# Optimization experiments

Hardware: AMD Instinct MI355X
Metric: run time of the kernel (lower is better)

## Reference

```python
import jax, jax.numpy as jnp
import numpy as np
from math import sqrt

BASE = 10000.0  # rope_theta
NUM_HEADS = 16


def _quant(x):
    # per-row (last-dim) symmetric int8 fake-quant, matching ActivationQuantSTE.forward
    scale = 127.0 / jnp.maximum(jnp.max(jnp.abs(x), axis=-1, keepdims=True), 1e-5)
    return jnp.clip(jnp.round(x * scale), -128.0, 127.0) / scale


@jax.custom_vjp
def act_quant(x):
    return _quant(x)

def _aq_fwd(x):
    return _quant(x), None

def _aq_bwd(_, g):
    return (g,)  # straight-through estimator

act_quant.defvjp(_aq_fwd, _aq_bwd)


def complex_linear(xr, xi, Wr, Wi):
    # ComplexLinearBase: quantize activations, then
    #   y_real = q_real @ Wr^T + q_imag @ Wi^T
    #   y_imag = q_real @ Wi^T - q_imag @ Wr^T
    qr = act_quant(xr)
    qi = act_quant(xi)
    yr = qr @ Wr.T + qi @ Wi.T
    yi = qr @ Wi.T - qi @ Wr.T
    return yr, yi


def setup_inputs() -> dict:
    T, H = 2048, 2048
    key = jax.random.key(0)
    ks = jax.random.split(key, 10)
    w = lambda k: jax.random.normal(k, (H, H), jnp.float32) * 0.02
    return {
        "hidden_real": jax.random.normal(ks[0], (T, H), jnp.float32),
        "hidden_imag": jax.random.normal(ks[1], (T, H), jnp.float32),
        "positions": jnp.arange(T, dtype=jnp.int32),
        "Wq_r": w(ks[2]), "Wq_i": w(ks[3]),
        "Wk_r": w(ks[4]), "Wk_i": w(ks[5]),
        "Wv_r": w(ks[6]), "Wv_i": w(ks[7]),
        "Wo_r": w(ks[8]), "Wo_i": w(ks[9]),
    }


def reference(hidden_real, hidden_imag, positions, Wq_r, Wq_i, Wk_r, Wk_i, Wv_r, Wv_i, Wo_r, Wo_i):
    T, H = hidden_real.shape
    NH = NUM_HEADS
    D = H // NH  # head_dim

    # complex QKV projections with int8 activation fake-quant
    qr, qi = complex_linear(hidden_real, hidden_imag, Wq_r, Wq_i)
    kr, ki = complex_linear(hidden_real, hidden_imag, Wk_r, Wk_i)
    vr, vi = complex_linear(hidden_real, hidden_imag, Wv_r, Wv_i)

    # Complex RoPE: interleaving (real, imag) then GPT-J-style rotation with
    # head_size = rotary_dim = 2*D is equivalent to rotating (real, imag) pairs:
    #   out_real = real*cos - imag*sin ; out_imag = imag*cos + real*sin
    # inv_freq = base^-(arange(0, 2D, 2)/(2D)) = base^-(arange(D)/D), len D.
    inv_freq = 1.0 / (BASE ** (jnp.arange(D, dtype=jnp.float32) / D))
    freqs = positions.astype(jnp.float32)[:, None] * inv_freq[None, :]  # [T, D]
    # cache is stored in bf16 in the original module
    cos = jnp.cos(freqs).astype(jnp.bfloat16).astype(jnp.float32)[:, None, :]  # [T,1,D]
    sin = jnp.sin(freqs).astype(jnp.bfloat16).astype(jnp.float32)[:, None, :]

    def rope(xr_, xi_):
        r = xr_.reshape(T, NH, D)
        i = xi_.reshape(T, NH, D)
        return r * cos - i * sin, i * cos + r * sin

    qr3, qi3 = rope(qr, qi)
    kr3, ki3 = rope(kr, ki)
    vr3 = vr.reshape(T, NH, D)
    vi3 = vi.reshape(T, NH, D)

    # causal attention; scores = Re(q . conj(k)) / sqrt(2*D)  (complex dim is 2*D)
    scale = 1.0 / sqrt(2 * D)
    scores = (jnp.einsum('thd,shd->hts', qr3, kr3)
              + jnp.einsum('thd,shd->hts', qi3, ki3)) * scale  # [NH, T, T]
    causal = jnp.tril(jnp.ones((T, T), dtype=bool))
    scores = jnp.where(causal[None], scores, -1e9)
    p = jax.nn.softmax(scores, axis=-1)

    out_r = jnp.einsum('hts,shd->thd', p, vr3).reshape(T, H)
    out_i = jnp.einsum('hts,shd->thd', p, vi3).reshape(T, H)

    # complex output projection (with activation fake-quant)
    return complex_linear(out_r, out_i, Wo_r, Wo_i)
```

## Files before the change

kernel.cpp:

```cpp
#include <hip/hip_runtime.h>


typedef float v4f __attribute__((ext_vector_type(4)));
typedef _Float16 v8h __attribute__((ext_vector_type(8)));
typedef _Float16 v4h __attribute__((ext_vector_type(4)));

typedef const __attribute__((address_space(1))) void glob_void;
typedef __attribute__((address_space(3))) void lds_void;

__device__ __forceinline__ void gload16(const _Float16* gp, _Float16* lp) {
  __builtin_amdgcn_global_load_lds((glob_void*)gp, (lds_void*)lp, 16, 0, 0);
}

__device__ __forceinline__ float bf16_rt(float f) {
  union { float f; unsigned u; } a; a.f = f;
  unsigned r = (a.u + 0x7fffu + ((a.u >> 16) & 1u)) & 0xffff0000u;
  union { unsigned u; float f; } b; b.u = r;
  return b.f;
}

#define EPI_QKV 0
#define EPI_OUT 1

#define SBAR()  __builtin_amdgcn_sched_barrier(0)
#define WBAR()  __builtin_amdgcn_s_barrier()
#define LGKM0() asm volatile("s_waitcnt lgkmcnt(0)" ::: "memory")
#define LDS_BARRIER() do { SBAR(); LGKM0(); WBAR(); SBAR(); } while (0)

__global__ __launch_bounds__(512, 2) void gemm_qkv256(
    const _Float16* __restrict__ A, const _Float16* __restrict__ B,
    _Float16* __restrict__ Yq, _Float16* __restrict__ vt)
{
  const int p = blockIdx.x;
  const int xcd = p & 7, s = p >> 3;
  const int mt = s & 7, ntl = s >> 3;
  const int nt = xcd * 8 + ntl;
  const int m0 = mt << 8;
  const int n0 = nt * 192;

  __shared__ __align__(16) _Float16 lds[57344];

  const int tid = threadIdx.x, lane = tid & 63, wave = tid >> 6;
  const int quad = lane >> 4, l15 = lane & 15;
  const int wm = wave >> 2, wn = wave & 3;

  const int rr = tid >> 2;
  const int lc8 = (((tid & 3) ^ ((tid >> 3) & 3)) << 3);
  const _Float16* gA = A + (long long)(m0 + rr) * 4096 + lc8;
  const _Float16* gBj[3];
#pragma unroll
  for (int j = 0; j < 3; ++j) {
    const int ks = (j == 2) || (j == 1 && tid >= 256);
    const int r = j * 128 + (tid >> 2) - ks * 192;
    gBj[j] = B + (long long)(n0 + r) * 4096 + ks * 32 + lc8;
  }

  const int co = ((quad ^ ((l15 >> 1) & 3)) << 3);
  const int aBase = (wm * 128 + l15) * 32 + co;
  const int bBase = (wn * 48 + l15) * 32 + co;

  v4f acc[8][3] = {};

  {
    _Float16* sd = lds + tid * 8;
    gload16(gA, sd);
    gload16(gA + 524288, sd + 4096);
    gload16(gBj[0], sd + 16384);
    gload16(gBj[1], sd + 20480);
    gload16(gA + 32, sd + 8192);
    gload16(gA + 524288 + 32, sd + 12288);
    gload16(gBj[2], sd + 24576);
  }
  asm volatile("s_waitcnt vmcnt(3)" ::: "memory");
  WBAR();

  for (int t = 0; t < 64; ++t) {
    const _Float16* As = lds + (t & 1) * 28672;
    const _Float16* Bs = As + 16384;
    _Float16* sd = lds + ((t & 1) ^ 1) * 28672 + tid * 8;
    const int k1 = (t + 1) << 6;
    const bool stg = (t < 63);

    v8h bf[3], af[4];

    af[0] = *(const v8h*)&As[aBase];
    af[1] = *(const v8h*)&As[aBase + 512];
    af[2] = *(const v8h*)&As[aBase + 1024];
    af[3] = *(const v8h*)&As[aBase + 1536];
    bf[0] = *(const v8h*)&Bs[bBase];
    bf[1] = *(const v8h*)&Bs[bBase + 512];
    bf[2] = *(const v8h*)&Bs[bBase + 1024];
    if (stg) { gload16(gA + k1, sd); gload16(gA + k1 + 524288, sd + 4096); }
    SBAR(); WBAR(); LGKM0(); SBAR();
    __builtin_amdgcn_s_setprio(1);
#pragma unroll
    for (int i = 0; i < 4; ++i)
#pragma unroll
      for (int nf = 0; nf < 3; ++nf)
        acc[i][nf] = __builtin_amdgcn_mfma_f32_16x16x32_f16(af[i], bf[nf], acc[i][nf], 0, 0, 0);
    __builtin_amdgcn_s_setprio(0);
    WBAR();

    af[0] = *(const v8h*)&As[aBase + 2048];
    af[1] = *(const v8h*)&As[aBase + 2560];
    af[2] = *(const v8h*)&As[aBase + 3072];
    af[3] = *(const v8h*)&As[aBase + 3584];
    if (stg) { gload16(gBj[0] + k1, sd + 16384); gload16(gBj[1] + k1, sd + 20480); }
    SBAR(); WBAR(); LGKM0(); SBAR();
    __builtin_amdgcn_s_setprio(1);
#pragma unroll
    for (int i = 0; i < 4; ++i)
#pragma unroll
      for (int nf = 0; nf < 3; ++nf)
        acc[4 + i][nf] = __builtin_amdgcn_mfma_f32_16x16x32_f16(af[i], bf[nf], acc[4 + i][nf], 0, 0, 0);
    __builtin_amdgcn_s_setprio(0);
    if (stg) asm volatile("s_waitcnt vmcnt(4)" ::: "memory");
    else     asm volatile("s_waitcnt vmcnt(0)" ::: "memory");
    WBAR();

    bf[0] = *(const v8h*)&Bs[bBase + 6144];
    bf[1] = *(const v8h*)&Bs[bBase + 6656];
    bf[2] = *(const v8h*)&Bs[bBase + 7168];
    af[0] = *(const v8h*)&As[aBase + 8192];
    af[1] = *(const v8h*)&As[aBase + 8704];
    af[2] = *(const v8h*)&As[aBase + 9216];
    af[3] = *(const v8h*)&As[aBase + 9728];
    if (stg) { gload16(gA + k1 + 32, sd + 8192); gload16(gA + k1 + 524288 + 32, sd + 12288); }
    SBAR(); WBAR(); LGKM0(); SBAR();
    __builtin_amdgcn_s_setprio(1);
#pragma unroll
    for (int i = 0; i < 4; ++i)
#pragma unroll
      for (int nf = 0; nf < 3; ++nf)
        acc[i][nf] = __builtin_amdgcn_mfma_f32_16x16x32_f16(af[i], bf[nf], acc[i][nf], 0, 0, 0);
    __builtin_amdgcn_s_setprio(0);
    WBAR();

    af[0] = *(const v8h*)&As[aBase + 10240];
    af[1] = *(const v8h*)&As[aBase + 10752];
    af[2] = *(const v8h*)&As[aBase + 11264];
    af[3] = *(const v8h*)&As[aBase + 11776];
    if (stg) gload16(gBj[2] + k1, sd + 24576);
    SBAR(); WBAR(); LGKM0(); SBAR();
    __builtin_amdgcn_s_setprio(1);
#pragma unroll
    for (int i = 0; i < 4; ++i)
#pragma unroll
      for (int nf = 0; nf < 3; ++nf)
        acc[4 + i][nf] = __builtin_amdgcn_mfma_f32_16x16x32_f16(af[i], bf[nf], acc[4 + i][nf], 0, 0, 0);
    __builtin_amdgcn_s_setprio(0);
    if (stg) asm volatile("s_waitcnt vmcnt(3)" ::: "memory");
    WBAR();
  }

#pragma unroll
  for (int mf = 0; mf < 8; ++mf) {
#pragma unroll
    for (int nf = 0; nf < 3; ++nf) {
      const int col = n0 + wn * 48 + nf * 16 + l15;
      const int row0 = m0 + wm * 128 + mf * 16 + quad * 4;
      if (col >= 8192) {
        const int c = col - 8192;
        const int hh = (c & 2047) >> 7;
        const int dcol = (c < 2048) ? (c & 127) : (128 + (c & 127));
        v4h pk;
#pragma unroll
        for (int r = 0; r < 4; ++r) pk[r] = (_Float16)acc[mf][nf][r];
        *(v4h*)(vt + ((long long)(hh * 256 + dcol)) * 2048 + row0) = pk;
      } else {
#pragma unroll
        for (int r = 0; r < 4; ++r)
          Yq[(long long)(row0 + r) * 8192 + col] = (_Float16)acc[mf][nf][r];
      }
    }
  }
}

template<int EPI>
__global__ __launch_bounds__(256) void gemm_nt(
    const _Float16* __restrict__ A, const _Float16* __restrict__ B,
    void* __restrict__ Cv, int K, int lda, int ldb, int ldc,
    _Float16* __restrict__ vtout)
{
  const int m0 = blockIdx.x * 128, n0 = blockIdx.y * 128;

  __shared__ __align__(16) _Float16 As[128 * 32];
  __shared__ __align__(16) _Float16 Bs[128 * 32];

  const int tid = threadIdx.x, lane = tid & 63, wave = tid >> 6;
  const int off0 = tid * 8, off1 = 2048 + tid * 8;
  const int r0 = off0 >> 5, r1 = off1 >> 5;
  const int c0 = ((((off0 >> 3) & 3) ^ ((r0 >> 1) & 3)) << 3);
  const int c1 = ((((off1 >> 3) & 3) ^ ((r1 >> 1) & 3)) << 3);
  const _Float16* ga0 = A + (long long)(m0 + r0) * lda + c0;
  const _Float16* ga1 = A + (long long)(m0 + r1) * lda + c1;
  const _Float16* gb0 = B + (long long)(n0 + r0) * ldb + c0;
  const _Float16* gb1 = B + (long long)(n0 + r1) * ldb + c1;

  const int mr = (wave >> 1) * 64 + (lane & 15);
  const int nr = (wave & 1) * 64 + (lane & 15);
  const int kq = lane >> 4;

  v4f acc[4][4] = {};

  for (int k0 = 0; k0 < K; k0 += 32) {
    gload16(ga0 + k0, As + off0);
    gload16(ga1 + k0, As + off1);
    gload16(gb0 + k0, Bs + off0);
    gload16(gb1 + k0, Bs + off1);
    __syncthreads();
    v8h a[4], b[4];
#pragma unroll
    for (int i = 0; i < 4; ++i) {
      const int r = mr + i * 16;
      a[i] = *(const v8h*)&As[r * 32 + ((kq ^ ((r >> 1) & 3)) << 3)];
    }
#pragma unroll
    for (int j = 0; j < 4; ++j) {
      const int r = nr + j * 16;
      b[j] = *(const v8h*)&Bs[r * 32 + ((kq ^ ((r >> 1) & 3)) << 3)];
    }
#pragma unroll
    for (int i = 0; i < 4; ++i)
#pragma unroll
      for (int j = 0; j < 4; ++j)
        acc[i][j] = __builtin_amdgcn_mfma_f32_16x16x32_f16(a[i], b[j], acc[i][j], 0, 0, 0);
    __syncthreads();
  }

  const int cr = (wave >> 1) * 64 + (lane >> 4) * 4;
  const int cc = (wave & 1) * 64 + (lane & 15);
#pragma unroll
  for (int i = 0; i < 4; ++i)
#pragma unroll
    for (int j = 0; j < 4; ++j) {
      const int col = n0 + cc + j * 16;
      if (EPI == EPI_QKV && col >= 8192) {
        const int c = col - 8192;
        const int hh = (c & 2047) >> 7;
        const int dcol = (c < 2048) ? (c & 127) : (128 + (c & 127));
        const int row0 = m0 + cr + i * 16;
        v4h pk;
#pragma unroll
        for (int r = 0; r < 4; ++r) pk[r] = (_Float16)acc[i][j][r];
        *(v4h*)(vtout + ((long long)(hh * 256 + dcol)) * 2048 + row0) = pk;
      } else {
#pragma unroll
        for (int r = 0; r < 4; ++r) {
          const int row = m0 + cr + i * 16 + r;
          const float v = acc[i][j][r];
          if (EPI == EPI_QKV) {
            ((_Float16*)Cv)[(long long)row * ldc + col] = (_Float16)v;
          } else {
            float* O = (float*)Cv;
            if (col < 2048) O[(long long)row * 2048 + col] = v;
            else O[2048ll * 2048 + (long long)row * 2048 + (col - 2048)] = v;
          }
        }
      }
    }
}

__global__ __launch_bounds__(256) void quant_rows(
    const float* __restrict__ s0, const float* __restrict__ s1,
    _Float16* __restrict__ dst)
{
  const int t = blockIdx.x, y = blockIdx.y;
  const float* src = (y ? s1 : s0) + (long long)t * 2048;
  const int tid = threadIdx.x, lane = tid & 63, wave = tid >> 6;
  __shared__ float rbuf[4];
  const v4f a = *(const v4f*)(src + tid * 4);
  const v4f b = *(const v4f*)(src + 1024 + tid * 4);
  float m = 0.f;
#pragma unroll
  for (int k = 0; k < 4; ++k)
    m = fmaxf(m, fmaxf(fabsf(a[k]), fabsf(b[k])));
  for (int o = 1; o < 64; o <<= 1) m = fmaxf(m, __shfl_xor(m, o, 64));
  if (lane == 0) rbuf[wave] = m;
  __syncthreads();
  m = fmaxf(fmaxf(rbuf[0], rbuf[1]), fmaxf(rbuf[2], rbuf[3]));
  const float scale = 127.f / fmaxf(m, 1e-5f);
  const float inv = 1.f / scale;
  _Float16* d = dst + (long long)t * 4096 + (long long)y * 2048 + tid * 4;
  v4h qa, qb;
#pragma unroll
  for (int k = 0; k < 4; ++k) {
    qa[k] = (_Float16)(fminf(fmaxf(rintf(a[k] * scale), -128.f), 127.f) * inv);
    qb[k] = (_Float16)(fminf(fmaxf(rintf(b[k] * scale), -128.f), 127.f) * inv);
  }
  *(v4h*)d = qa;
  *(v4h*)(d + 1024) = qb;
}

__global__ __launch_bounds__(256) void wprep(
    const float* __restrict__ Wq_r, const float* __restrict__ Wq_i,
    const float* __restrict__ Wk_r, const float* __restrict__ Wk_i,
    const float* __restrict__ Wv_r, const float* __restrict__ Wv_i,
    const float* __restrict__ Wo_r, const float* __restrict__ Wo_i,
    _Float16* __restrict__ Bqkv, _Float16* __restrict__ Bo)
{
  const float* Ws[8] = {Wq_r, Wq_i, Wk_r, Wk_i, Wv_r, Wv_i, Wo_r, Wo_i};
  const int i = blockIdx.x * 256 + threadIdx.x;
  const int w = i >> 18;
  const int rem = i & 262143;
  const int j = rem >> 7;
  const int cb = (rem & 127) * 16;
  const float* src = Ws[w] + (long long)j * 2048 + cb;
  _Float16* Bp = (w < 6) ? (Bqkv + (long long)(w >> 1) * 4096 * 4096) : Bo;
  const int isI = w & 1;
  _Float16* d1 = Bp + (long long)j * 4096 + (isI ? 2048 + cb : cb);
  _Float16* d2 = Bp + (long long)(2048 + j) * 4096 + (isI ? cb : 2048 + cb);
  const float sg2 = isI ? 1.f : -1.f;
#pragma unroll
  for (int q = 0; q < 4; ++q) {
    const v4f v = *(const v4f*)(src + q * 4);
    v4h o1, o2;
#pragma unroll
    for (int k = 0; k < 4; ++k) {
      o1[k] = (_Float16)v[k];
      o2[k] = (_Float16)(v[k] * sg2);
    }
    *(v4h*)(d1 + q * 4) = o1;
    *(v4h*)(d2 + q * 4) = o2;
  }
}

__global__ __launch_bounds__(256) void trig_kernel(
    const int* __restrict__ pos, float* __restrict__ cs)
{
  const int t = blockIdx.x * 2 + (threadIdx.x >> 7);
  const int d = threadIdx.x & 127;
  const float invf = (float)pow(10000.0, -(double)d / 128.0);
  const float fr = (float)pos[t] * invf;
  const double fd = (double)fr;
  cs[((long long)t * 128 + d) * 2]     = bf16_rt((float)cos(fd));
  cs[((long long)t * 128 + d) * 2 + 1] = bf16_rt((float)sin(fd));
}

__global__ __launch_bounds__(256) void rope_kernel(
    const _Float16* __restrict__ Yq, const float* __restrict__ cs,
    _Float16* __restrict__ qc, _Float16* __restrict__ kc)
{
  const int idx = blockIdx.x * 256 + threadIdx.x;
  const int d0 = (idx & 15) * 8;
  const int h  = (idx >> 4) & 15;
  const int t  = idx >> 8;
  const _Float16* y = Yq + (long long)t * 8192 + h * 128 + d0;
  const v8h qr8 = *(const v8h*)(y);
  const v8h qi8 = *(const v8h*)(y + 2048);
  const v8h kr8 = *(const v8h*)(y + 4096);
  const v8h ki8 = *(const v8h*)(y + 6144);
  const float* cp = cs + ((long long)t * 128 + d0) * 2;
  v8h qro, qio, kro, kio;
#pragma unroll
  for (int u = 0; u < 8; ++u) {
    const float c = cp[u * 2], s = cp[u * 2 + 1];
    const float qr = (float)qr8[u], qi = (float)qi8[u];
    const float kr = (float)kr8[u], ki = (float)ki8[u];
    qro[u] = (_Float16)(qr * c - qi * s);
    qio[u] = (_Float16)(qi * c + qr * s);
    kro[u] = (_Float16)(kr * c - ki * s);
    kio[u] = (_Float16)(ki * c + kr * s);
  }
  _Float16* qo = qc + ((long long)h * 2048 + t) * 256 + d0;
  _Float16* ko = kc + ((long long)h * 2048 + t) * 256 + d0;
  *(v8h*)qo = qro; *(v8h*)(qo + 128) = qio;
  *(v8h*)ko = kro; *(v8h*)(ko + 128) = kio;
}

__global__ __launch_bounds__(256, 2) void flash_attn(
    const _Float16* __restrict__ qc, const _Float16* __restrict__ kc,
    const _Float16* __restrict__ vt, float* __restrict__ attn)
{
  __shared__ __align__(16) _Float16 Ps[64 * 72];
  __shared__ float pmax[2][64];
  __shared__ float psum[2][64];

  const int h  = blockIdx.y;
  const int qt = ((h >> 3) & 1) ? (31 - (int)blockIdx.x) : (int)blockIdx.x;
  const int q0 = qt * 64;
  const int tid = threadIdx.x, lane = tid & 63, wave = tid >> 6;
  const int mi = wave >> 1, ni = wave & 1;
  const int quad = lane >> 4, l15 = lane & 15;

  const _Float16* qh = qc + (long long)h * 2048 * 256;
  const _Float16* kh = kc + (long long)h * 2048 * 256;
  const _Float16* vh = vt + (long long)h * 256 * 2048;

  const _Float16 scl = (_Float16)0.09016844f;
  v8h qf[2][8];
#pragma unroll
  for (int mt = 0; mt < 2; ++mt) {
    const int t = q0 + mi * 32 + mt * 16 + l15;
#pragma unroll
    for (int ks = 0; ks < 8; ++ks) {
      v8h q = *(const v8h*)(qh + (long long)t * 256 + ks * 32 + quad * 8);
#pragma unroll
      for (int u = 0; u < 8; ++u) q[u] *= scl;
      qf[mt][ks] = q;
    }
  }

  float mrow[2][4], lrow[2][4];
  v4f acc_o[2][8];
#pragma unroll
  for (int mt = 0; mt < 2; ++mt)
#pragma unroll
    for (int r = 0; r < 4; ++r) { mrow[mt][r] = -1e30f; lrow[mt][r] = 0.f; }
#pragma unroll
  for (int mt = 0; mt < 2; ++mt)
#pragma unroll
    for (int nt = 0; nt < 8; ++nt) acc_o[mt][nt] = (v4f){0.f, 0.f, 0.f, 0.f};

  for (int st = 0; st <= qt; ++st) {
    const int s0 = st * 64;

    v4f sa[2][2] = {};
#pragma unroll
    for (int ks = 0; ks < 8; ++ks) {
      v8h bk[2];
#pragma unroll
      for (int jn = 0; jn < 2; ++jn)
        bk[jn] = *(const v8h*)(kh + (long long)(s0 + ni * 32 + jn * 16 + l15) * 256
                               + ks * 32 + quad * 8);
      __builtin_amdgcn_s_setprio(1);
#pragma unroll
      for (int mt = 0; mt < 2; ++mt)
#pragma unroll
        for (int jn = 0; jn < 2; ++jn)
          sa[mt][jn] = __builtin_amdgcn_mfma_f32_16x16x32_f16(qf[mt][ks], bk[jn], sa[mt][jn], 0, 0, 0);
      __builtin_amdgcn_s_setprio(0);
    }

    const bool diag = (st == qt);
    float pm[2][4];
#pragma unroll
    for (int mt = 0; mt < 2; ++mt)
#pragma unroll
      for (int r = 0; r < 4; ++r) pm[mt][r] = -1e30f;
#pragma unroll
    for (int mt = 0; mt < 2; ++mt)
#pragma unroll
      for (int jn = 0; jn < 2; ++jn)
#pragma unroll
        for (int r = 0; r < 4; ++r) {
          float v = sa[mt][jn][r];
          if (diag) {
            const int rl = mi * 32 + mt * 16 + quad * 4 + r;
            const int cl = ni * 32 + jn * 16 + l15;
            if (cl > rl) v = -1e30f;
          }
          sa[mt][jn][r] = v;
          pm[mt][r] = fmaxf(pm[mt][r], v);
        }
#pragma unroll
    for (int o = 1; o < 16; o <<= 1)
#pragma unroll
      for (int mt = 0; mt < 2; ++mt)
#pragma unroll
        for (int r = 0; r < 4; ++r)
          pm[mt][r] = fmaxf(pm[mt][r], __shfl_xor(pm[mt][r], o, 64));
    if (l15 == 0) {
#pragma unroll
      for (int mt = 0; mt < 2; ++mt)
#pragma unroll
        for (int r = 0; r < 4; ++r)
          pmax[ni][mi * 32 + mt * 16 + quad * 4 + r] = pm[mt][r];
    }
    LDS_BARRIER();

    float al[2][4], ps[2][4];
#pragma unroll
    for (int mt = 0; mt < 2; ++mt)
#pragma unroll
      for (int r = 0; r < 4; ++r) {
        const int row = mi * 32 + mt * 16 + quad * 4 + r;
        const float mn = fmaxf(mrow[mt][r], fmaxf(pmax[0][row], pmax[1][row]));
        al[mt][r] = __builtin_amdgcn_exp2f(mrow[mt][r] - mn);
        mrow[mt][r] = mn;
        ps[mt][r] = 0.f;
      }
#pragma unroll
    for (int mt = 0; mt < 2; ++mt)
#pragma unroll
      for (int jn = 0; jn < 2; ++jn)
#pragma unroll
        for (int r = 0; r < 4; ++r) {
          const float e = __builtin_amdgcn_exp2f(sa[mt][jn][r] - mrow[mt][r]);
          ps[mt][r] += e;
          Ps[(mi * 32 + mt * 16 + quad * 4 + r) * 72 + ni * 32 + jn * 16 + l15] = (_Float16)e;
        }
#pragma unroll
    for (int o = 1; o < 16; o <<= 1)
#pragma unroll
      for (int mt = 0; mt < 2; ++mt)
#pragma unroll
        for (int r = 0; r < 4; ++r)
          ps[mt][r] += __shfl_xor(ps[mt][r], o, 64);
    if (l15 == 0) {
#pragma unroll
      for (int mt = 0; mt < 2; ++mt)
#pragma unroll
        for (int r = 0; r < 4; ++r)
          psum[ni][mi * 32 + mt * 16 + quad * 4 + r] = ps[mt][r];
    }
    LDS_BARRIER();

#pragma unroll
    for (int mt = 0; mt < 2; ++mt)
#pragma unroll
      for (int r = 0; r < 4; ++r) {
        const int row = mi * 32 + mt * 16 + quad * 4 + r;
        lrow[mt][r] = lrow[mt][r] * al[mt][r] + psum[0][row] + psum[1][row];
      }
#pragma unroll
    for (int mt = 0; mt < 2; ++mt)
#pragma unroll
      for (int nt = 0; nt < 8; ++nt)
#pragma unroll
        for (int r = 0; r < 4; ++r)
          acc_o[mt][nt][r] *= al[mt][r];

#pragma unroll
    for (int kc2 = 0; kc2 < 2; ++kc2) {
      v8h pa[2];
#pragma unroll
      for (int mt = 0; mt < 2; ++mt) {
        const int row = mi * 32 + mt * 16 + l15;
        pa[mt] = *(const v8h*)(Ps + row * 72 + kc2 * 32 + quad * 8);
      }
#pragma unroll
      for (int nt = 0; nt < 8; ++nt) {
        const v8h vb = *(const v8h*)(vh + (long long)(ni * 128 + nt * 16 + l15) * 2048
                                     + s0 + kc2 * 32 + quad * 8);
        __builtin_amdgcn_s_setprio(1);
#pragma unroll
        for (int mt = 0; mt < 2; ++mt)
          acc_o[mt][nt] = __builtin_amdgcn_mfma_f32_16x16x32_f16(pa[mt], vb, acc_o[mt][nt], 0, 0, 0);
        __builtin_amdgcn_s_setprio(0);
      }
    }
  }

#pragma unroll
  for (int mt = 0; mt < 2; ++mt) {
    float inv[4];
#pragma unroll
    for (int r = 0; r < 4; ++r) inv[r] = 1.f / lrow[mt][r];
#pragma unroll
    for (int nt = 0; nt < 8; ++nt) {
      const int d = ni * 128 + nt * 16 + l15;
      float* dst = attn + ((d < 128) ? 0ll : (2048ll * 2048)) + (h * 128 + (d & 127));
#pragma unroll
      for (int r = 0; r < 4; ++r) {
        const int t = q0 + mi * 32 + mt * 16 + quad * 4 + r;
        dst[(long long)t * 2048] = acc_o[mt][nt][r] * inv[r];
      }
    }
  }
}

extern "C" void kernel_launch(void* const* d_in, const int* in_sizes, int n_in,
                              void* d_out, int out_size, void* d_ws, size_t ws_size,
                              hipStream_t stream) {
  const float* hr   = (const float*)d_in[0];
  const float* hi   = (const float*)d_in[1];
  const int*   pos  = (const int*)d_in[2];
  const float* Wq_r = (const float*)d_in[3];
  const float* Wq_i = (const float*)d_in[4];
  const float* Wk_r = (const float*)d_in[5];
  const float* Wk_i = (const float*)d_in[6];
  const float* Wv_r = (const float*)d_in[7];
  const float* Wv_i = (const float*)d_in[8];
  const float* Wo_r = (const float*)d_in[9];
  const float* Wo_i = (const float*)d_in[10];

  char* ws = (char*)d_ws;
  _Float16* Bqkv = (_Float16*)(ws);
  float*    attn = (float*)   (ws);
  float*    cs   = (float*)   (ws + (32ll  << 20));
  _Float16* Bo   = (_Float16*)(ws + (96ll  << 20));
  _Float16* Ac   = (_Float16*)(ws + (128ll << 20));
  _Float16* Yq   = (_Float16*)(ws + (144ll << 20));
  _Float16* qc   = (_Float16*)(ws + (176ll << 20));
  _Float16* kc   = (_Float16*)(ws + (192ll << 20));
  _Float16* vt   = (_Float16*)(ws + (208ll << 20));

  quant_rows<<<dim3(2048, 2), 256, 0, stream>>>(hr, hi, Ac);
  wprep<<<8192, 256, 0, stream>>>(Wq_r, Wq_i, Wk_r, Wk_i, Wv_r, Wv_i, Wo_r, Wo_i, Bqkv, Bo);
  gemm_qkv256<<<512, 512, 0, stream>>>(Ac, Bqkv, Yq, vt);
  trig_kernel<<<1024, 256, 0, stream>>>(pos, cs);
  rope_kernel<<<2048, 256, 0, stream>>>(Yq, cs, qc, kc);
  flash_attn<<<dim3(32, 16), 256, 0, stream>>>(qc, kc, vt, attn);
  quant_rows<<<dim3(2048, 2), 256, 0, stream>>>(attn, attn + 2048ll * 2048, Ac);
  gemm_nt<EPI_OUT><<<dim3(16, 32), 256, 0, stream>>>(
      Ac, Bo, d_out, 4096, 4096, 4096, 0, nullptr);
}
```

Baseline: 774.1 us.

## Replace output GEMM with double-buffered 256x128 pipelined kernel, simplify attention sync

Replaces the simple single-buffered 128x128 output projection GEMM with a 512-thread, 256x128-tile kernel. It double-buffers LDS and issues async global-to-LDS loads interleaved with MFMA phases, and maps blocks with XCD-aware ordering. This is meant to hide memory latency and improve reuse in the K=4096 output GEMM. Separately, attention drops the s_setprio hints and its custom barrier macro in favour of __syncthreads, which may slightly change scheduling.

```diff
diff --git a/kernel.cpp b/kernel.cpp
--- a/kernel.cpp
+++ b/kernel.cpp
@@ -19,13 +19,9 @@
   return b.f;
 }
 
-#define EPI_QKV 0
-#define EPI_OUT 1
-
 #define SBAR()  __builtin_amdgcn_sched_barrier(0)
 #define WBAR()  __builtin_amdgcn_s_barrier()
 #define LGKM0() asm volatile("s_waitcnt lgkmcnt(0)" ::: "memory")
-#define LDS_BARRIER() do { SBAR(); LGKM0(); WBAR(); SBAR(); } while (0)
 
 __global__ __launch_bounds__(512, 2) void gemm_qkv256(
     const _Float16* __restrict__ A, const _Float16* __restrict__ B,
@@ -176,89 +172,137 @@
   }
 }
 
-template<int EPI>
-__global__ __launch_bounds__(256) void gemm_nt(
+__global__ __launch_bounds__(512, 2) void gemm_out256(
     const _Float16* __restrict__ A, const _Float16* __restrict__ B,
-    void* __restrict__ Cv, int K, int lda, int ldb, int ldc,
-    _Float16* __restrict__ vtout)
+    float* __restrict__ O)
 {
-  const int m0 = blockIdx.x * 128, n0 = blockIdx.y * 128;
-
-  __shared__ __align__(16) _Float16 As[128 * 32];
-  __shared__ __align__(16) _Float16 Bs[128 * 32];
+  const int p = blockIdx.x;
+  const int xcd = p & 7, s = p >> 3;
+  const int mt = s & 7, ntl = s >> 3;
+  const int nt = xcd * 4 + ntl;
+  const int m0 = mt << 8, n0 = nt << 7;
+
+  __shared__ __align__(16) _Float16 lds[49152];
 
   const int tid = threadIdx.x, lane = tid & 63, wave = tid >> 6;
-  const int off0 = tid * 8, off1 = 2048 + tid * 8;
-  const int r0 = off0 >> 5, r1 = off1 >> 5;
-  const int c0 = ((((off0 >> 3) & 3) ^ ((r0 >> 1) & 3)) << 3);
-  const int c1 = ((((off1 >> 3) & 3) ^ ((r1 >> 1) & 3)) << 3);
-  const _Float16* ga0 = A + (long long)(m0 + r0) * lda + c0;
-  const _Float16* ga1 = A + (long long)(m0 + r1) * lda + c1;
-  const _Float16* gb0 = B + (long long)(n0 + r0) * ldb + c0;
-  const _Float16* gb1 = B + (long long)(n0 + r1) * ldb + c1;
-
-  const int mr = (wave >> 1) * 64 + (lane & 15);
-  const int nr = (wave & 1) * 64 + (lane & 15);
-  const int kq = lane >> 4;
-
-  v4f acc[4][4] = {};
-
-  for (int k0 = 0; k0 < K; k0 += 32) {
-    gload16(ga0 + k0, As + off0);
-    gload16(ga1 + k0, As + off1);
-    gload16(gb0 + k0, Bs + off0);
-    gload16(gb1 + k0, Bs + off1);
-    __syncthreads();
-    v8h a[4], b[4];
-#pragma unroll
-    for (int i = 0; i < 4; ++i) {
-      const int r = mr + i * 16;
-      a[i] = *(const v8h*)&As[r * 32 + ((kq ^ ((r >> 1) & 3)) << 3)];
-    }
-#pragma unroll
-    for (int j = 0; j < 4; ++j) {
-      const int r = nr + j * 16;
-      b[j] = *(const v8h*)&Bs[r * 32 + ((kq ^ ((r >> 1) & 3)) << 3)];
-    }
-#pragma unroll
-    for (int i = 0; i < 4; ++i)
-#pragma unroll
-      for (int j = 0; j < 4; ++j)
-        acc[i][j] = __builtin_amdgcn_mfma_f32_16x16x32_f16(a[i], b[j], acc[i][j], 0, 0, 0);
-    __syncthreads();
-  }
-
-  const int cr = (wave >> 1) * 64 + (lane >> 4) * 4;
-  const int cc = (wave & 1) * 64 + (lane & 15);
-#pragma unroll
-  for (int i = 0; i < 4; ++i)
-#pragma unroll
-    for (int j = 0; j < 4; ++j) {
-      const int col = n0 + cc + j * 16;
-      if (EPI == EPI_QKV && col >= 8192) {
-        const int c = col - 8192;
-        const int hh = (c & 2047) >> 7;
-        const int dcol = (c < 2048) ? (c & 127) : (128 + (c & 127));
-        const int row0 = m0 + cr + i * 16;
-        v4h pk;
-#pragma unroll
-        for (int r = 0; r < 4; ++r) pk[r] = (_Float16)acc[i][j][r];
-        *(v4h*)(vtout + ((long long)(hh * 256 + dcol)) * 2048 + row0) = pk;
-      } else {
-#pragma unroll
-        for (int r = 0; r < 4; ++r) {
-          const int row = m0 + cr + i * 16 + r;
-          const float v = acc[i][j][r];
-          if (EPI == EPI_QKV) {
-            ((_Float16*)Cv)[(long long)row * ldc + col] = (_Float16)v;
-          } else {
-            float* O = (float*)Cv;
-            if (col < 2048) O[(long long)row * 2048 + col] = v;
-            else O[2048ll * 2048 + (long long)row * 2048 + (col - 2048)] = v;
-          }
-        }
+  const int quad = lane >> 4, l15 = lane & 15;
+  const int wm = wave >> 2, wn = wave & 3;
+
+  const int rr = tid >> 2;
+  const int lc8 = (((tid & 3) ^ ((tid >> 3) & 3)) << 3);
+  const _Float16* gA = A + (long long)(m0 + rr) * 4096 + lc8;
+  const _Float16* gB = B + (long long)(n0 + rr) * 4096 + lc8;
+
+  const int co = ((quad ^ ((l15 >> 1) & 3)) << 3);
+  const int aBase = (wm * 128 + l15) * 32 + co;
+  const int bBase = (wn * 32 + l15) * 32 + co;
+
+  v4f acc[8][2] = {};
+
+  {
+    _Float16* sd = lds + tid * 8;
+    gload16(gA, sd);
+    gload16(gA + 524288, sd + 4096);
+    gload16(gB, sd + 16384);
+    gload16(gA + 32, sd + 8192);
+    gload16(gA + 524288 + 32, sd + 12288);
+    gload16(gB + 32, sd + 20480);
+  }
+  asm volatile("s_waitcnt vmcnt(3)" ::: "memory");
+  WBAR();
+
+  for (int t = 0; t < 64; ++t) {
+    const _Float16* As = lds + (t & 1) * 24576;
+    const _Float16* Bs = As + 16384;
+    _Float16* sd = lds + ((t & 1) ^ 1) * 24576 + tid * 8;
+    const int k1 = (t + 1) << 6;
+    const bool stg = (t < 63);
+
+    v8h bf[2], af[4];
+
+    af[0] = *(const v8h*)&As[aBase];
+    af[1] = *(const v8h*)&As[aBase + 512];
+    af[2] = *(const v8h*)&As[aBase + 1024];
+    af[3] = *(const v8h*)&As[aBase + 1536];
+    bf[0] = *(const v8h*)&Bs[bBase];
+    bf[1] = *(const v8h*)&Bs[bBase + 512];
+    if (stg) { gload16(gA + k1, sd); gload16(gA + k1 + 524288, sd + 4096); }
+    SBAR(); WBAR(); LGKM0(); SBAR();
+    __builtin_amdgcn_s_setprio(1);
+#pragma unroll
+    for (int i = 0; i < 4; ++i)
+#pragma unroll
+      for (int nf = 0; nf < 2; ++nf)
+        acc[i][nf] = __builtin_amdgcn_mfma_f32_16x16x32_f16(af[i], bf[nf], acc[i][nf], 0, 0, 0);
+    __builtin_amdgcn_s_setprio(0);
+    WBAR();
+
+    af[0] = *(const v8h*)&As[aBase + 2048];
+    af[1] = *(const v8h*)&As[aBase + 2560];
+    af[2] = *(const v8h*)&As[aBase + 3072];
+    af[3] = *(const v8h*)&As[aBase + 3584];
+    if (stg) gload16(gB + k1, sd + 16384);
+    SBAR(); WBAR(); LGKM0(); SBAR();
+    __builtin_amdgcn_s_setprio(1);
+#pragma unroll
+    for (int i = 0; i < 4; ++i)
+#pragma unroll
+      for (int nf = 0; nf < 2; ++nf)
+        acc[4 + i][nf] = __builtin_amdgcn_mfma_f32_16x16x32_f16(af[i], bf[nf], acc[4 + i][nf], 0, 0, 0);
+    __builtin_amdgcn_s_setprio(0);
+    if (stg) asm volatile("s_waitcnt vmcnt(3)" ::: "memory");
+    else     asm volatile("s_waitcnt vmcnt(0)" ::: "memory");
+    WBAR();
+
+    bf[0] = *(const v8h*)&Bs[bBase + 4096];
+    bf[1] = *(const v8h*)&Bs[bBase + 4608];
+    af[0] = *(const v8h*)&As[aBase + 8192];
+    af[1] = *(const v8h*)&As[aBase + 8704];
+    af[2] = *(const v8h*)&As[aBase + 9216];
+    af[3] = *(const v8h*)&As[aBase + 9728];
+    if (stg) { gload16(gA + k1 + 32, sd + 8192); gload16(gA + k1 + 524288 + 32, sd + 12288); }
+    SBAR(); WBAR(); LGKM0(); SBAR();
+    __builtin_amdgcn_s_setprio(1);
+#pragma unroll
+    for (int i = 0; i < 4; ++i)
+#pragma unroll
+      for (int nf = 0; nf < 2; ++nf)
+        acc[i][nf] = __builtin_amdgcn_mfma_f32_16x16x32_f16(af[i], bf[nf], acc[i][nf], 0, 0, 0);
+    __builtin_amdgcn_s_setprio(0);
+    WBAR();
+
+    af[0] = *(const v8h*)&As[aBase + 10240];
+    af[1] = *(const v8h*)&As[aBase + 10752];
+    af[2] = *(const v8h*)&As[aBase + 11264];
+    af[3] = *(const v8h*)&As[aBase + 11776];
+    if (stg) gload16(gB + k1 + 32, sd + 20480);
+    SBAR(); WBAR(); LGKM0(); SBAR();
+    __builtin_amdgcn_s_setprio(1);
+#pragma unroll
+    for (int i = 0; i < 4; ++i)
+#pragma unroll
+      for (int nf = 0; nf < 2; ++nf)
+        acc[4 + i][nf] = __builtin_amdgcn_mfma_f32_16x16x32_f16(af[i], bf[nf], acc[4 + i][nf], 0, 0, 0);
+    __builtin_amdgcn_s_setprio(0);
+    if (stg) asm volatile("s_waitcnt vmcnt(3)" ::: "memory");
+    WBAR();
+  }
+
+#pragma unroll
+  for (int mf = 0; mf < 8; ++mf) {
+#pragma unroll
+    for (int nf = 0; nf < 2; ++nf) {
+      const int col = n0 + wn * 32 + nf * 16 + l15;
+      const int row0 = m0 + wm * 128 + mf * 16 + quad * 4;
+#pragma unroll
+      for (int r = 0; r < 4; ++r) {
+        const int row = row0 + r;
+        const float v = acc[mf][nf][r];
+        if (col < 2048) O[(long long)row * 2048 + col] = v;
+        else O[2048ll * 2048 + (long long)row * 2048 + (col - 2048)] = v;
       }
     }
+  }
 }
 
 __global__ __launch_bounds__(256) void quant_rows(
@@ -423,13 +467,11 @@
       for (int jn = 0; jn < 2; ++jn)
         bk[jn] = *(const v8h*)(kh + (long long)(s0 + ni * 32 + jn * 16 + l15) * 256
                                + ks * 32 + quad * 8);
-      __builtin_amdgcn_s_setprio(1);
 #pragma unroll
       for (int mt = 0; mt < 2; ++mt)
 #pragma unroll
         for (int jn = 0; jn < 2; ++jn)
           sa[mt][jn] = __builtin_amdgcn_mfma_f32_16x16x32_f16(qf[mt][ks], bk[jn], sa[mt][jn], 0, 0, 0);
-      __builtin_amdgcn_s_setprio(0);
     }
 
     const bool diag = (st == qt);
@@ -467,7 +509,7 @@
         for (int r = 0; r < 4; ++r)
           pmax[ni][mi * 32 + mt * 16 + quad * 4 + r] = pm[mt][r];
     }
-    LDS_BARRIER();
+    __syncthreads();
 
     float al[2][4], ps[2][4];
 #pragma unroll
@@ -504,7 +546,7 @@
         for (int r = 0; r < 4; ++r)
           psum[ni][mi * 32 + mt * 16 + quad * 4 + r] = ps[mt][r];
     }
-    LDS_BARRIER();
+    __syncthreads();
 
 #pragma unroll
     for (int mt = 0; mt < 2; ++mt)
@@ -533,11 +575,9 @@
       for (int nt = 0; nt < 8; ++nt) {
         const v8h vb = *(const v8h*)(vh + (long long)(ni * 128 + nt * 16 + l15) * 2048
                                      + s0 + kc2 * 32 + quad * 8);
-        __builtin_amdgcn_s_setprio(1);
 #pragma unroll
         for (int mt = 0; mt < 2; ++mt)
           acc_o[mt][nt] = __builtin_amdgcn_mfma_f32_16x16x32_f16(pa[mt], vb, acc_o[mt][nt], 0, 0, 0);
-        __builtin_amdgcn_s_setprio(0);
       }
     }
   }
@@ -593,6 +633,5 @@
   rope_kernel<<<2048, 256, 0, stream>>>(Yq, cs, qc, kc);
   flash_attn<<<dim3(32, 16), 256, 0, stream>>>(qc, kc, vt, attn);
   quant_rows<<<dim3(2048, 2), 256, 0, stream>>>(attn, attn + 2048ll * 2048, Ac);
-  gemm_nt<EPI_OUT><<<dim3(16, 32), 256, 0, stream>>>(
-      Ac, Bo, d_out, 4096, 4096, 4096, 0, nullptr);
-}
+  gemm_out256<<<256, 512, 0, stream>>>(Ac, Bo, (float*)d_out);
+}
```

Measured after the change: 701.8 us. 1.1x faster.
